# Performance work log

Hardware: AMD Instinct MI355X
Metric: run time of the kernel (lower is better)

## Reference

```python
import jax, jax.numpy as jnp
import numpy as np

N = 100000
E = 1600000
EPS = 1e-5


def setup_inputs() -> dict:
    key = jax.random.key(0)
    ks = jax.random.split(key, 6)
    x = jax.random.normal(ks[0], (N, 128), dtype=jnp.float32)
    edge_index = jax.random.randint(ks[1], (2, E), 0, N, dtype=jnp.int64)
    # Glorot-ish scaled weights
    W1 = jax.random.normal(ks[2], (128, 128), dtype=jnp.float32) * (1.0 / np.sqrt(128))
    b1 = jnp.zeros((128,), dtype=jnp.float32)
    gamma = jnp.ones((128,), dtype=jnp.float32)
    beta = jnp.zeros((128,), dtype=jnp.float32)
    W2 = jax.random.normal(ks[3], (64, 128), dtype=jnp.float32) * (1.0 / np.sqrt(128))
    b2 = jnp.zeros((64,), dtype=jnp.float32)
    return {"x": x, "edge_index": edge_index, "W1": W1, "b1": b1,
            "gamma": gamma, "beta": beta, "W2": W2, "b2": b2}


def _gcn_conv(x, W, b, src, dst, norm, n):
    # x: [N, Fin], W: [Fout, Fin] -> h: [N, Fout]
    h = x @ W.T
    msg = h[src] * norm[:, None]               # [E+N, Fout] gather + scale
    out = jax.ops.segment_sum(msg, dst, num_segments=n)  # scatter-add
    return out + b


def reference(x, edge_index, W1, b1, gamma, beta, W2, b2):
    n = x.shape[0]
    loop = jnp.arange(n, dtype=edge_index.dtype)
    src = jnp.concatenate([edge_index[0], loop])   # self-loops appended
    dst = jnp.concatenate([edge_index[1], loop])
    # symmetric normalization D^-1/2 A D^-1/2 (degree at destination)
    deg = jax.ops.segment_sum(jnp.ones_like(dst, dtype=x.dtype), dst, num_segments=n)
    dis = jnp.where(deg > 0, jax.lax.rsqrt(deg), 0.0)
    norm = dis[src] * dis[dst]

    h = _gcn_conv(x, W1, b1, src, dst, norm, n)
    # BatchNorm1d (training mode: biased batch statistics over nodes)
    mean = jnp.mean(h, axis=0)
    var = jnp.mean((h - mean) ** 2, axis=0)
    h = (h - mean) * jax.lax.rsqrt(var + EPS) * gamma + beta
    h = jax.nn.relu(h)
    out = _gcn_conv(h, W2, b2, src, dst, norm, n)
    return out
```

## Files before the change

kernel.cpp:

```cpp
#include <hip/hip_runtime.h>


#define SHIFT 8
#define BSZ   256
#define CHUNK 4096
#define EPT   (CHUNK/256)
#define NBMAX 1024

typedef short bf16x8 __attribute__((ext_vector_type(8)));
typedef float f32x4  __attribute__((ext_vector_type(4)));

__device__ __forceinline__ unsigned short f2bf(float f) {
    unsigned int u = __float_as_uint(f);
    unsigned int r = (u + 0x7FFFu + ((u >> 16) & 1u)) >> 16;
    return (unsigned short)r;
}
__device__ __forceinline__ float bf2f(unsigned short h) {
    return __uint_as_float(((unsigned int)h) << 16);
}
__device__ __forceinline__ unsigned int pack2bf(float a, float b) {
    return (unsigned int)f2bf(a) | ((unsigned int)f2bf(b) << 16);
}
__device__ __forceinline__ void fma4(float4& acc, float s, const float4& w) {
    acc.x += s * w.x; acc.y += s * w.y; acc.z += s * w.z; acc.w += s * w.w;
}

__device__ __forceinline__ void split2(float a, float b, unsigned int& hi, unsigned int& lo) {
    unsigned int ua = __float_as_uint(a), ub = __float_as_uint(b);
    unsigned int ha = ua & 0xFFFF0000u,  hb = ub & 0xFFFF0000u;
    hi = (ha >> 16) | hb;
    float la = a - __uint_as_float(ha);
    float lb = b - __uint_as_float(hb);
    lo = (__float_as_uint(la) >> 16) | (__float_as_uint(lb) & 0xFFFF0000u);
}

__global__ void k_detect(const int* __restrict__ ei32, int* __restrict__ flag) {
    if (threadIdx.x == 0 && blockIdx.x == 0) {
        int o = 0;
        for (int q = 0; q < 16; ++q) o |= ei32[2 * q + 1];
        flag[0] = (o == 0) ? 1 : 0;
    }
}

__global__ __launch_bounds__(256) void k_hist(const void* __restrict__ eiv,
                                              const int* __restrict__ flag,
                                              int* __restrict__ gcnt,
                                              int E, int N, int NB) {
    __shared__ int h[NBMAX];
    int t = threadIdx.x;
    for (int u = t; u < NB; u += 256) h[u] = 0;
    __syncthreads();
    int base = blockIdx.x * CHUNK;
    int f = flag[0];
    const long long* e64 = (const long long*)eiv;
    const int*       e32 = (const int*)eiv;
#pragma unroll
    for (int r = 0; r < EPT; ++r) {
        int e = base + r * 256 + t;
        if (e < E) {
            int s, d;
            if (f) { s = (int)e64[e]; d = (int)e64[E + e]; }
            else   { s = e32[e];      d = e32[E + e]; }
            if ((unsigned)s < (unsigned)N && (unsigned)d < (unsigned)N)
                atomicAdd(&h[d >> SHIFT], 1);
        }
    }
    __syncthreads();
    for (int u = t; u < NB; u += 256) {
        int c = h[u];
        if (c) atomicAdd(&gcnt[u], c);
    }
}

__global__ void k_scan(const int* __restrict__ gcnt, int* __restrict__ gbase,
                       int* __restrict__ gcur, int NB) {
    __shared__ int sh[1024];
    int t = threadIdx.x;
    int v = (t < NB) ? gcnt[t] : 0;
    sh[t] = v;
    __syncthreads();
    for (int off = 1; off < 1024; off <<= 1) {
        int x = sh[t];
        int y = (t >= off) ? sh[t - off] : 0;
        __syncthreads();
        sh[t] = x + y;
        __syncthreads();
    }
    if (t < NB) {
        int ex = sh[t] - v;
        gbase[t] = ex;
        gcur[t]  = ex;
    }
    if (t == 0) gbase[NB] = sh[1023];
}

__global__ __launch_bounds__(256) void k_scatter(const void* __restrict__ eiv,
                                                 const int* __restrict__ flag,
                                                 int* __restrict__ gcur,
                                                 unsigned int* __restrict__ ebuf,
                                                 int E, int N, int NB) {
    __shared__ int lcnt[NBMAX];
    __shared__ int lbase[NBMAX];
    int t = threadIdx.x;
    for (int u = t; u < NB; u += 256) lcnt[u] = 0;
    __syncthreads();
    int base = blockIdx.x * CHUNK;
    int f = flag[0];
    const long long* e64 = (const long long*)eiv;
    const int*       e32 = (const int*)eiv;
    unsigned int ent[EPT];
    int bk[EPT];
    int off[EPT];
#pragma unroll
    for (int r = 0; r < EPT; ++r) {
        int e = base + r * 256 + t;
        bk[r] = -1;
        if (e < E) {
            int s, d;
            if (f) { s = (int)e64[e]; d = (int)e64[E + e]; }
            else   { s = e32[e];      d = e32[E + e]; }
            if ((unsigned)s < (unsigned)N && (unsigned)d < (unsigned)N) {
                int b = d >> SHIFT;
                bk[r]  = b;
                off[r] = atomicAdd(&lcnt[b], 1);
                ent[r] = ((unsigned int)(d & (BSZ - 1)) << 24) | (unsigned int)s;
            }
        }
    }
    __syncthreads();
    for (int u = t; u < NB; u += 256) {
        int c = lcnt[u];
        lbase[u] = c ? atomicAdd(&gcur[u], c) : 0;
    }
    __syncthreads();
#pragma unroll
    for (int r = 0; r < EPT; ++r)
        if (bk[r] >= 0) ebuf[(size_t)lbase[bk[r]] + off[r]] = ent[r];
}

__global__ __launch_bounds__(256) void k_fine(const unsigned int* __restrict__ ebuf,
                                              const int* __restrict__ gbase,
                                              int* __restrict__ cnt,
                                              float* __restrict__ dis,
                                              int* __restrict__ rowptr,
                                              int* __restrict__ elist, int N) {
    __shared__ int lc[BSZ];
    __shared__ int ls[BSZ];
    int t = threadIdx.x;
    int b = blockIdx.x;
    int start = gbase[b], end = gbase[b + 1];
    int m = end - start;
    lc[t] = 0;
    __syncthreads();
    for (int j = t; j < m; j += 256)
        atomicAdd(&lc[ebuf[start + j] >> 24], 1);
    __syncthreads();
    int v = lc[t];
    ls[t] = v;
    __syncthreads();
    for (int off = 1; off < BSZ; off <<= 1) {
        int x = ls[t];
        int y = (t >= off) ? ls[t - off] : 0;
        __syncthreads();
        ls[t] = x + y;
        __syncthreads();
    }
    int ex = ls[t] - v;
    int i = (b << SHIFT) + t;
    if (i < N) {
        cnt[i]    = v;
        dis[i]    = rsqrtf((float)v + 1.0f);
        rowptr[i] = start + ex;
    }
    lc[t] = ex;
    __syncthreads();
    for (int j = t; j < m; j += 256) {
        unsigned int e = ebuf[start + j];
        int p = atomicAdd(&lc[e >> 24], 1);
        elist[start + p] = (int)(e & 0xFFFFFFu);
    }
}

__global__ __launch_bounds__(256) void k_transpose(const float* __restrict__ src,
                                                   float* __restrict__ dst, int O) {
    int idx = blockIdx.x * 256 + threadIdx.x;
    if (idx >= O * 128) return;
    int k = idx & 127, o = idx >> 7;
    dst[k * O + o] = src[o * 128 + k];
}

__global__ __launch_bounds__(256) void k_prepw(const float* __restrict__ W,
                                               uint4* __restrict__ Whi,
                                               uint4* __restrict__ Wlo, int NT) {
    int idx = blockIdx.x * 256 + threadIdx.x;
    if (idx >= NT * 4 * 64) return;
    int lane = idx & 63, kt = (idx >> 6) & 3, nt = idx >> 8;
    int o = nt * 16 + (lane & 15);
    int k0 = kt * 32 + (lane >> 4) * 8;
    const float* p = W + (size_t)o * 128 + k0;
    unsigned int h[4], l[4];
#pragma unroll
    for (int pr = 0; pr < 4; ++pr) split2(p[2 * pr], p[2 * pr + 1], h[pr], l[pr]);
    Whi[idx] = make_uint4(h[0], h[1], h[2], h[3]);
    Wlo[idx] = make_uint4(l[0], l[1], l[2], l[3]);
}

__global__ __launch_bounds__(256) void k_gemm1(const float* __restrict__ x,
                                               const uint4* __restrict__ Whi,
                                               const uint4* __restrict__ Wlo,
                                               const float* __restrict__ dis,
                                               unsigned short* __restrict__ h1b, int N) {
    __shared__ uint4 Ahi[1024];
    __shared__ uint4 Alo[1024];
    int t = threadIdx.x;
    int n0 = blockIdx.x * 64;
    for (int s = t; s < 1024; s += 256) {
        int lane = s & 63, kt = (s >> 6) & 3, c = s >> 8;
        int row = n0 + c * 16 + (lane & 15);
        int rr = min(row, N - 1);
        int k0 = kt * 32 + (lane >> 4) * 8;
        const float4* p = (const float4*)(x + (size_t)rr * 128 + k0);
        float4 u0 = p[0], u1 = p[1];
        unsigned int h0, h1, h2, h3, l0, l1, l2, l3;
        split2(u0.x, u0.y, h0, l0);
        split2(u0.z, u0.w, h1, l1);
        split2(u1.x, u1.y, h2, l2);
        split2(u1.z, u1.w, h3, l3);
        Ahi[s] = make_uint4(h0, h1, h2, h3);
        Alo[s] = make_uint4(l0, l1, l2, l3);
    }
    __syncthreads();
    int w = t >> 6, lane = t & 63;
    bf16x8 ah[4], al[4];
#pragma unroll
    for (int kt = 0; kt < 4; ++kt) {
        ah[kt] = ((const bf16x8*)Ahi)[(w * 4 + kt) * 64 + lane];
        al[kt] = ((const bf16x8*)Alo)[(w * 4 + kt) * 64 + lane];
    }
    f32x4 acc[8];
#pragma unroll
    for (int nt = 0; nt < 8; ++nt) {
        acc[nt] = (f32x4)(0.f);
#pragma unroll
        for (int kt = 0; kt < 4; ++kt) {
            bf16x8 bh = ((const bf16x8*)Whi)[(nt * 4 + kt) * 64 + lane];
            bf16x8 bl = ((const bf16x8*)Wlo)[(nt * 4 + kt) * 64 + lane];
            acc[nt] = __builtin_amdgcn_mfma_f32_16x16x32_bf16(ah[kt], bh, acc[nt], 0, 0, 0);
            acc[nt] = __builtin_amdgcn_mfma_f32_16x16x32_bf16(ah[kt], bl, acc[nt], 0, 0, 0);
            acc[nt] = __builtin_amdgcn_mfma_f32_16x16x32_bf16(al[kt], bh, acc[nt], 0, 0, 0);
        }
    }
    int r0 = n0 + w * 16 + (lane >> 4) * 4;
    float dv[4];
#pragma unroll
    for (int r = 0; r < 4; ++r) {
        int row = r0 + r;
        dv[r] = (row < N) ? dis[row] : 0.f;
    }
#pragma unroll
    for (int nt = 0; nt < 8; ++nt) {
        int col = nt * 16 + (lane & 15);
#pragma unroll
        for (int r = 0; r < 4; ++r) {
            int row = r0 + r;
            if (row < N) h1b[(size_t)row * 128 + col] = f2bf(dv[r] * acc[nt][r]);
        }
    }
}

__global__ __launch_bounds__(256) void k_agg1(const unsigned int* __restrict__ h1b,
                                              const float* __restrict__ dis,
                                              const int* __restrict__ rowptr,
                                              const int* __restrict__ cnt,
                                              const int* __restrict__ elist,
                                              float* __restrict__ agg1, int N) {
    int lane = threadIdx.x & 63;
    int i = blockIdx.x * 4 + (threadIdx.x >> 6);
    if (i >= N) return;
    float accx = 0.f, accy = 0.f;
    int base = rowptr[i], c = cnt[i];
    int j = 0;
    for (; j + 8 <= c; j += 8) {
        int ss[8];
#pragma unroll
        for (int r = 0; r < 8; ++r) ss[r] = elist[base + j + r];
        unsigned int vv[8];
#pragma unroll
        for (int r = 0; r < 8; ++r) vv[r] = h1b[(size_t)ss[r] * 64 + lane];
#pragma unroll
        for (int r = 0; r < 8; ++r) {
            accx += bf2f((unsigned short)(vv[r] & 0xFFFF));
            accy += bf2f((unsigned short)(vv[r] >> 16));
        }
    }
    for (; j < c; ++j) {
        int s = elist[base + j];
        unsigned int v = h1b[(size_t)s * 64 + lane];
        accx += bf2f((unsigned short)(v & 0xFFFF));
        accy += bf2f((unsigned short)(v >> 16));
    }
    float di = dis[i];
    unsigned int sv = h1b[(size_t)i * 64 + lane];
    float2 r;
    r.x = di * (accx + bf2f((unsigned short)(sv & 0xFFFF)));
    r.y = di * (accy + bf2f((unsigned short)(sv >> 16)));
    ((float2*)agg1)[(size_t)i * 64 + lane] = r;
}

__global__ __launch_bounds__(256) void k_bnstats(const float* __restrict__ agg1,
                                                 float* __restrict__ stats, int N) {
    int t = threadIdx.x;
    int f = t & 127, half = t >> 7;
    float s = 0.f, sq = 0.f;
    int stride = gridDim.x * 2;
    for (int r = blockIdx.x * 2 + half; r < N; r += stride) {
        float v = agg1[r * 128 + f];
        s += v; sq += v * v;
    }
    __shared__ float ls[256], lq[256];
    ls[t] = s; lq[t] = sq;
    __syncthreads();
    if (t < 128) {
        atomicAdd(&stats[f], ls[t] + ls[t + 128]);
        atomicAdd(&stats[128 + f], lq[t] + lq[t + 128]);
    }
}

__global__ void k_bnfin(float* __restrict__ stats, const float* __restrict__ gamma,
                        const float* __restrict__ beta, int N) {
    int f = threadIdx.x;
    if (f >= 128) return;
    float invN = 1.0f / (float)N;
    float mean = stats[f] * invN;
    float var = stats[128 + f] * invN - mean * mean;
    var = fmaxf(var, 0.f);
    float inv = rsqrtf(var + 1e-5f);
    float sc = gamma[f] * inv;
    stats[256 + f] = sc;
    stats[384 + f] = beta[f] - mean * sc;
}

__global__ __launch_bounds__(256) void k_gemm2(const float* __restrict__ agg1,
                                               const float* __restrict__ WT2,
                                               const float* __restrict__ stats,
                                               const float* __restrict__ dis,
                                               uint2* __restrict__ h2b, int N) {
    int t = threadIdx.x;
    int q = t & 15, g = t >> 4;
    int n0 = blockIdx.x * 64 + g * 4;
    int m0 = min(n0 + 0, N - 1), m1 = min(n0 + 1, N - 1);
    int m2 = min(n0 + 2, N - 1), m3 = min(n0 + 3, N - 1);
    const float4* ar0 = (const float4*)agg1 + (size_t)m0 * 32;
    const float4* ar1 = (const float4*)agg1 + (size_t)m1 * 32;
    const float4* ar2 = (const float4*)agg1 + (size_t)m2 * 32;
    const float4* ar3 = (const float4*)agg1 + (size_t)m3 * 32;
    const float4* wt = (const float4*)WT2;
    const float4* st = (const float4*)stats;
    float4 acc0 = make_float4(0.f, 0.f, 0.f, 0.f), acc1 = acc0, acc2 = acc0, acc3 = acc0;
    for (int kq = 0; kq < 32; ++kq) {
        float4 sc = st[64 + kq], sh = st[96 + kq];
        float4 a0 = ar0[kq], a1 = ar1[kq], a2 = ar2[kq], a3 = ar3[kq];
        float4 r0, r1, r2, r3;
        r0.x = fmaxf(a0.x * sc.x + sh.x, 0.f); r0.y = fmaxf(a0.y * sc.y + sh.y, 0.f);
        r0.z = fmaxf(a0.z * sc.z + sh.z, 0.f); r0.w = fmaxf(a0.w * sc.w + sh.w, 0.f);
        r1.x = fmaxf(a1.x * sc.x + sh.x, 0.f); r1.y = fmaxf(a1.y * sc.y + sh.y, 0.f);
        r1.z = fmaxf(a1.z * sc.z + sh.z, 0.f); r1.w = fmaxf(a1.w * sc.w + sh.w, 0.f);
        r2.x = fmaxf(a2.x * sc.x + sh.x, 0.f); r2.y = fmaxf(a2.y * sc.y + sh.y, 0.f);
        r2.z = fmaxf(a2.z * sc.z + sh.z, 0.f); r2.w = fmaxf(a2.w * sc.w + sh.w, 0.f);
        r3.x = fmaxf(a3.x * sc.x + sh.x, 0.f); r3.y = fmaxf(a3.y * sc.y + sh.y, 0.f);
        r3.z = fmaxf(a3.z * sc.z + sh.z, 0.f); r3.w = fmaxf(a3.w * sc.w + sh.w, 0.f);
        float4 w0 = wt[(4 * kq + 0) * 16 + q];
        float4 w1 = wt[(4 * kq + 1) * 16 + q];
        float4 w2 = wt[(4 * kq + 2) * 16 + q];
        float4 w3 = wt[(4 * kq + 3) * 16 + q];
        fma4(acc0, r0.x, w0); fma4(acc0, r0.y, w1); fma4(acc0, r0.z, w2); fma4(acc0, r0.w, w3);
        fma4(acc1, r1.x, w0); fma4(acc1, r1.y, w1); fma4(acc1, r1.z, w2); fma4(acc1, r1.w, w3);
        fma4(acc2, r2.x, w0); fma4(acc2, r2.y, w1); fma4(acc2, r2.z, w2); fma4(acc2, r2.w, w3);
        fma4(acc3, r3.x, w0); fma4(acc3, r3.y, w1); fma4(acc3, r3.z, w2); fma4(acc3, r3.w, w3);
    }
    float d0 = dis[m0], d1 = dis[m1], d2 = dis[m2], d3 = dis[m3];
    if (n0 + 0 < N) h2b[(size_t)(n0 + 0) * 16 + q] = make_uint2(pack2bf(d0 * acc0.x, d0 * acc0.y), pack2bf(d0 * acc0.z, d0 * acc0.w));
    if (n0 + 1 < N) h2b[(size_t)(n0 + 1) * 16 + q] = make_uint2(pack2bf(d1 * acc1.x, d1 * acc1.y), pack2bf(d1 * acc1.z, d1 * acc1.w));
    if (n0 + 2 < N) h2b[(size_t)(n0 + 2) * 16 + q] = make_uint2(pack2bf(d2 * acc2.x, d2 * acc2.y), pack2bf(d2 * acc2.z, d2 * acc2.w));
    if (n0 + 3 < N) h2b[(size_t)(n0 + 3) * 16 + q] = make_uint2(pack2bf(d3 * acc3.x, d3 * acc3.y), pack2bf(d3 * acc3.z, d3 * acc3.w));
}

__global__ __launch_bounds__(256) void k_agg2(const unsigned short* __restrict__ h2b,
                                              const float* __restrict__ dis,
                                              const int* __restrict__ rowptr,
                                              const int* __restrict__ cnt,
                                              const int* __restrict__ elist,
                                              const float* __restrict__ b2,
                                              float* __restrict__ out, int N) {
    int lane = threadIdx.x & 63;
    int i = blockIdx.x * 4 + (threadIdx.x >> 6);
    if (i >= N) return;
    float acc = 0.f;
    int base = rowptr[i], c = cnt[i];
    int j = 0;
    for (; j + 8 <= c; j += 8) {
        int ss[8];
#pragma unroll
        for (int r = 0; r < 8; ++r) ss[r] = elist[base + j + r];
        unsigned short vv[8];
#pragma unroll
        for (int r = 0; r < 8; ++r) vv[r] = h2b[(size_t)ss[r] * 64 + lane];
#pragma unroll
        for (int r = 0; r < 8; ++r) acc += bf2f(vv[r]);
    }
    for (; j < c; ++j) {
        int s = elist[base + j];
        acc += bf2f(h2b[(size_t)s * 64 + lane]);
    }
    float di = dis[i];
    float self = bf2f(h2b[(size_t)i * 64 + lane]);
    out[(size_t)i * 64 + lane] = di * (acc + self) + b2[lane];
}

extern "C" void kernel_launch(void* const* d_in, const int* in_sizes, int n_in,
                              void* d_out, int out_size, void* d_ws, size_t ws_size,
                              hipStream_t stream) {
    const float* x     = (const float*)d_in[0];
    const void*  ei    = d_in[1];
    const float* W1    = (const float*)d_in[2];
    const float* gamma = (const float*)d_in[4];
    const float* beta  = (const float*)d_in[5];
    const float* W2    = (const float*)d_in[6];
    const float* b2    = (const float*)d_in[7];
    float* out = (float*)d_out;

    int N = in_sizes[0] / 128;
    int E = in_sizes[1] / 2;
    int NB = (N + BSZ - 1) >> SHIFT;

    size_t Na = ((size_t)N + 3) & ~(size_t)3;
    size_t Ea = ((size_t)E + 3) & ~(size_t)3;
    int*   cnt    = (int*)d_ws;
    int*   rowptr = cnt + Na;
    int*   gcnt   = rowptr + Na;
    int*   gbase  = gcnt + 1024;
    int*   gcur   = gbase + 1028;
    int*   flagA  = gcur + 1024;
    float* stats  = (float*)(flagA + 4);
    float* dis    = stats + 512;
    int*   elist  = (int*)(dis + Na);
    unsigned int* h1b = (unsigned int*)(elist + Ea);
    float* agg1   = (float*)(h1b + Na * 64);
    unsigned int* ebuf = (unsigned int*)agg1;
    float* WT2    = agg1 + Na * 128;
    uint4* Whi1   = (uint4*)(WT2 + 128 * 64);
    uint4* Wlo1   = Whi1 + 2048;
    unsigned int* h2b = h1b;

    hipMemsetAsync(gcnt, 0, 1024 * sizeof(int), stream);
    hipMemsetAsync(stats, 0, 512 * sizeof(float), stream);

    k_detect<<<1, 64, 0, stream>>>((const int*)ei, flagA);

    int gC    = (E + CHUNK - 1) / CHUNK;
    int gG1   = (N + 63) / 64;
    int gG2   = (N + 63) / 64;
    int gAgg  = (N + 3) / 4;

    k_prepw<<<8, 256, 0, stream>>>(W1, Whi1, Wlo1, 8);
    k_transpose<<<32, 256, 0, stream>>>(W2, WT2, 64);
    k_hist<<<gC, 256, 0, stream>>>(ei, flagA, gcnt, E, N, NB);
    k_scan<<<1, 1024, 0, stream>>>(gcnt, gbase, gcur, NB);
    k_scatter<<<gC, 256, 0, stream>>>(ei, flagA, gcur, ebuf, E, N, NB);
    k_fine<<<NB, 256, 0, stream>>>(ebuf, gbase, cnt, dis, rowptr, elist, N);
    k_gemm1<<<gG1, 256, 0, stream>>>(x, Whi1, Wlo1, dis, (unsigned short*)h1b, N);
    k_agg1<<<gAgg, 256, 0, stream>>>(h1b, dis, rowptr, cnt, elist, agg1, N);
    k_bnstats<<<500, 256, 0, stream>>>(agg1, stats, N);
    k_bnfin<<<1, 128, 0, stream>>>(stats, gamma, beta, N);
    k_gemm2<<<gG2, 256, 0, stream>>>(agg1, WT2, stats, dis, (uint2*)h2b, N);
    k_agg2<<<gAgg, 256, 0, stream>>>((const unsigned short*)h2b, dis, rowptr, cnt, elist, b2, out, N);
}
```

Baseline: 459.3 us.

## Move second GEMM to split-bf16 MFMA and unroll aggregation gathers by 16

Replaces the scalar FP32 second GEMM with a bf16 MFMA version that stages BN+ReLU-applied activations into shared memory as hi/lo bf16 splits. It reuses the prepw weight-split kernel for W2 and computes three MFMAs per tile to keep near-FP32 accuracy. Both aggregation kernels now issue 16 independent gathers per iteration instead of 8, to raise memory-level parallelism. The cost is extra register pressure, more shared memory per block, and the overhead of the hi/lo split.

Measured after the change: 418.4 us. 1.1x faster.

```diff
diff --git a/kernel.cpp b/kernel.cpp
--- a/kernel.cpp
+++ b/kernel.cpp
@@ -18,13 +18,6 @@
 __device__ __forceinline__ float bf2f(unsigned short h) {
     return __uint_as_float(((unsigned int)h) << 16);
 }
-__device__ __forceinline__ unsigned int pack2bf(float a, float b) {
-    return (unsigned int)f2bf(a) | ((unsigned int)f2bf(b) << 16);
-}
-__device__ __forceinline__ void fma4(float4& acc, float s, const float4& w) {
-    acc.x += s * w.x; acc.y += s * w.y; acc.z += s * w.z; acc.w += s * w.w;
-}
-
 __device__ __forceinline__ void split2(float a, float b, unsigned int& hi, unsigned int& lo) {
     unsigned int ua = __float_as_uint(a), ub = __float_as_uint(b);
     unsigned int ha = ua & 0xFFFF0000u,  hb = ub & 0xFFFF0000u;
@@ -179,14 +172,6 @@
         int p = atomicAdd(&lc[e >> 24], 1);
         elist[start + p] = (int)(e & 0xFFFFFFu);
     }
-}
-
-__global__ __launch_bounds__(256) void k_transpose(const float* __restrict__ src,
-                                                   float* __restrict__ dst, int O) {
-    int idx = blockIdx.x * 256 + threadIdx.x;
-    if (idx >= O * 128) return;
-    int k = idx & 127, o = idx >> 7;
-    dst[k * O + o] = src[o * 128 + k];
 }
 
 __global__ __launch_bounds__(256) void k_prepw(const float* __restrict__ W,
@@ -280,7 +265,20 @@
     float accx = 0.f, accy = 0.f;
     int base = rowptr[i], c = cnt[i];
     int j = 0;
-    for (; j + 8 <= c; j += 8) {
+    for (; j + 16 <= c; j += 16) {
+        int ss[16];
+#pragma unroll
+        for (int r = 0; r < 16; ++r) ss[r] = elist[base + j + r];
+        unsigned int vv[16];
+#pragma unroll
+        for (int r = 0; r < 16; ++r) vv[r] = h1b[(size_t)ss[r] * 64 + lane];
+#pragma unroll
+        for (int r = 0; r < 16; ++r) {
+            accx += bf2f((unsigned short)(vv[r] & 0xFFFF));
+            accy += bf2f((unsigned short)(vv[r] >> 16));
+        }
+    }
+    if (j + 8 <= c) {
         int ss[8];
 #pragma unroll
         for (int r = 0; r < 8; ++r) ss[r] = elist[base + j + r];
@@ -292,6 +290,7 @@
             accx += bf2f((unsigned short)(vv[r] & 0xFFFF));
             accy += bf2f((unsigned short)(vv[r] >> 16));
         }
+        j += 8;
     }
     for (; j < c; ++j) {
         int s = elist[base + j];
@@ -341,48 +340,78 @@
 }
 
 __global__ __launch_bounds__(256) void k_gemm2(const float* __restrict__ agg1,
-                                               const float* __restrict__ WT2,
+                                               const uint4* __restrict__ Whi,
+                                               const uint4* __restrict__ Wlo,
                                                const float* __restrict__ stats,
                                                const float* __restrict__ dis,
-                                               uint2* __restrict__ h2b, int N) {
-    int t = threadIdx.x;
-    int q = t & 15, g = t >> 4;
-    int n0 = blockIdx.x * 64 + g * 4;
-    int m0 = min(n0 + 0, N - 1), m1 = min(n0 + 1, N - 1);
-    int m2 = min(n0 + 2, N - 1), m3 = min(n0 + 3, N - 1);
-    const float4* ar0 = (const float4*)agg1 + (size_t)m0 * 32;
-    const float4* ar1 = (const float4*)agg1 + (size_t)m1 * 32;
-    const float4* ar2 = (const float4*)agg1 + (size_t)m2 * 32;
-    const float4* ar3 = (const float4*)agg1 + (size_t)m3 * 32;
-    const float4* wt = (const float4*)WT2;
+                                               unsigned short* __restrict__ h2b, int N) {
+    __shared__ uint4 Ahi[1024];
+    __shared__ uint4 Alo[1024];
+    int t = threadIdx.x;
+    int n0 = blockIdx.x * 64;
     const float4* st = (const float4*)stats;
-    float4 acc0 = make_float4(0.f, 0.f, 0.f, 0.f), acc1 = acc0, acc2 = acc0, acc3 = acc0;
-    for (int kq = 0; kq < 32; ++kq) {
-        float4 sc = st[64 + kq], sh = st[96 + kq];
-        float4 a0 = ar0[kq], a1 = ar1[kq], a2 = ar2[kq], a3 = ar3[kq];
-        float4 r0, r1, r2, r3;
-        r0.x = fmaxf(a0.x * sc.x + sh.x, 0.f); r0.y = fmaxf(a0.y * sc.y + sh.y, 0.f);
-        r0.z = fmaxf(a0.z * sc.z + sh.z, 0.f); r0.w = fmaxf(a0.w * sc.w + sh.w, 0.f);
-        r1.x = fmaxf(a1.x * sc.x + sh.x, 0.f); r1.y = fmaxf(a1.y * sc.y + sh.y, 0.f);
-        r1.z = fmaxf(a1.z * sc.z + sh.z, 0.f); r1.w = fmaxf(a1.w * sc.w + sh.w, 0.f);
-        r2.x = fmaxf(a2.x * sc.x + sh.x, 0.f); r2.y = fmaxf(a2.y * sc.y + sh.y, 0.f);
-        r2.z = fmaxf(a2.z * sc.z + sh.z, 0.f); r2.w = fmaxf(a2.w * sc.w + sh.w, 0.f);
-        r3.x = fmaxf(a3.x * sc.x + sh.x, 0.f); r3.y = fmaxf(a3.y * sc.y + sh.y, 0.f);
-        r3.z = fmaxf(a3.z * sc.z + sh.z, 0.f); r3.w = fmaxf(a3.w * sc.w + sh.w, 0.f);
-        float4 w0 = wt[(4 * kq + 0) * 16 + q];
-        float4 w1 = wt[(4 * kq + 1) * 16 + q];
-        float4 w2 = wt[(4 * kq + 2) * 16 + q];
-        float4 w3 = wt[(4 * kq + 3) * 16 + q];
-        fma4(acc0, r0.x, w0); fma4(acc0, r0.y, w1); fma4(acc0, r0.z, w2); fma4(acc0, r0.w, w3);
-        fma4(acc1, r1.x, w0); fma4(acc1, r1.y, w1); fma4(acc1, r1.z, w2); fma4(acc1, r1.w, w3);
-        fma4(acc2, r2.x, w0); fma4(acc2, r2.y, w1); fma4(acc2, r2.z, w2); fma4(acc2, r2.w, w3);
-        fma4(acc3, r3.x, w0); fma4(acc3, r3.y, w1); fma4(acc3, r3.z, w2); fma4(acc3, r3.w, w3);
-    }
-    float d0 = dis[m0], d1 = dis[m1], d2 = dis[m2], d3 = dis[m3];
-    if (n0 + 0 < N) h2b[(size_t)(n0 + 0) * 16 + q] = make_uint2(pack2bf(d0 * acc0.x, d0 * acc0.y), pack2bf(d0 * acc0.z, d0 * acc0.w));
-    if (n0 + 1 < N) h2b[(size_t)(n0 + 1) * 16 + q] = make_uint2(pack2bf(d1 * acc1.x, d1 * acc1.y), pack2bf(d1 * acc1.z, d1 * acc1.w));
-    if (n0 + 2 < N) h2b[(size_t)(n0 + 2) * 16 + q] = make_uint2(pack2bf(d2 * acc2.x, d2 * acc2.y), pack2bf(d2 * acc2.z, d2 * acc2.w));
-    if (n0 + 3 < N) h2b[(size_t)(n0 + 3) * 16 + q] = make_uint2(pack2bf(d3 * acc3.x, d3 * acc3.y), pack2bf(d3 * acc3.z, d3 * acc3.w));
+    for (int s = t; s < 1024; s += 256) {
+        int lane = s & 63, kt = (s >> 6) & 3, c = s >> 8;
+        int row = n0 + c * 16 + (lane & 15);
+        int rr = min(row, N - 1);
+        int k0 = kt * 32 + (lane >> 4) * 8;
+        const float4* p = (const float4*)(agg1 + (size_t)rr * 128 + k0);
+        float4 a0 = p[0], a1 = p[1];
+        float4 c0 = st[64 + (k0 >> 2)], c1 = st[65 + (k0 >> 2)];
+        float4 s0 = st[96 + (k0 >> 2)], s1 = st[97 + (k0 >> 2)];
+        float v0 = fmaxf(a0.x * c0.x + s0.x, 0.f);
+        float v1 = fmaxf(a0.y * c0.y + s0.y, 0.f);
+        float v2 = fmaxf(a0.z * c0.z + s0.z, 0.f);
+        float v3 = fmaxf(a0.w * c0.w + s0.w, 0.f);
+        float v4 = fmaxf(a1.x * c1.x + s1.x, 0.f);
+        float v5 = fmaxf(a1.y * c1.y + s1.y, 0.f);
+        float v6 = fmaxf(a1.z * c1.z + s1.z, 0.f);
+        float v7 = fmaxf(a1.w * c1.w + s1.w, 0.f);
+        unsigned int h0, h1, h2, h3, l0, l1, l2, l3;
+        split2(v0, v1, h0, l0);
+        split2(v2, v3, h1, l1);
+        split2(v4, v5, h2, l2);
+        split2(v6, v7, h3, l3);
+        Ahi[s] = make_uint4(h0, h1, h2, h3);
+        Alo[s] = make_uint4(l0, l1, l2, l3);
+    }
+    __syncthreads();
+    int w = t >> 6, lane = t & 63;
+    bf16x8 ah[4], al[4];
+#pragma unroll
+    for (int kt = 0; kt < 4; ++kt) {
+        ah[kt] = ((const bf16x8*)Ahi)[(w * 4 + kt) * 64 + lane];
+        al[kt] = ((const bf16x8*)Alo)[(w * 4 + kt) * 64 + lane];
+    }
+    f32x4 acc[4];
+#pragma unroll
+    for (int nt = 0; nt < 4; ++nt) {
+        acc[nt] = (f32x4)(0.f);
+#pragma unroll
+        for (int kt = 0; kt < 4; ++kt) {
+            bf16x8 bh = ((const bf16x8*)Whi)[(nt * 4 + kt) * 64 + lane];
+            bf16x8 bl = ((const bf16x8*)Wlo)[(nt * 4 + kt) * 64 + lane];
+            acc[nt] = __builtin_amdgcn_mfma_f32_16x16x32_bf16(ah[kt], bh, acc[nt], 0, 0, 0);
+            acc[nt] = __builtin_amdgcn_mfma_f32_16x16x32_bf16(ah[kt], bl, acc[nt], 0, 0, 0);
+            acc[nt] = __builtin_amdgcn_mfma_f32_16x16x32_bf16(al[kt], bh, acc[nt], 0, 0, 0);
+        }
+    }
+    int r0 = n0 + w * 16 + (lane >> 4) * 4;
+    float dv[4];
+#pragma unroll
+    for (int r = 0; r < 4; ++r) {
+        int row = r0 + r;
+        dv[r] = (row < N) ? dis[row] : 0.f;
+    }
+#pragma unroll
+    for (int nt = 0; nt < 4; ++nt) {
+        int col = nt * 16 + (lane & 15);
+#pragma unroll
+        for (int r = 0; r < 4; ++r) {
+            int row = r0 + r;
+            if (row < N) h2b[(size_t)row * 64 + col] = f2bf(dv[r] * acc[nt][r]);
+        }
+    }
 }
 
 __global__ __launch_bounds__(256) void k_agg2(const unsigned short* __restrict__ h2b,
@@ -398,7 +427,17 @@
     float acc = 0.f;
     int base = rowptr[i], c = cnt[i];
     int j = 0;
-    for (; j + 8 <= c; j += 8) {
+    for (; j + 16 <= c; j += 16) {
+        int ss[16];
+#pragma unroll
+        for (int r = 0; r < 16; ++r) ss[r] = elist[base + j + r];
+        unsigned short vv[16];
+#pragma unroll
+        for (int r = 0; r < 16; ++r) vv[r] = h2b[(size_t)ss[r] * 64 + lane];
+#pragma unroll
+        for (int r = 0; r < 16; ++r) acc += bf2f(vv[r]);
+    }
+    if (j + 8 <= c) {
         int ss[8];
 #pragma unroll
         for (int r = 0; r < 8; ++r) ss[r] = elist[base + j + r];
@@ -407,6 +446,7 @@
         for (int r = 0; r < 8; ++r) vv[r] = h2b[(size_t)ss[r] * 64 + lane];
 #pragma unroll
         for (int r = 0; r < 8; ++r) acc += bf2f(vv[r]);
+        j += 8;
     }
     for (; j < c; ++j) {
         int s = elist[base + j];
@@ -447,9 +487,10 @@
     unsigned int* h1b = (unsigned int*)(elist + Ea);
     float* agg1   = (float*)(h1b + Na * 64);
     unsigned int* ebuf = (unsigned int*)agg1;
-    float* WT2    = agg1 + Na * 128;
-    uint4* Whi1   = (uint4*)(WT2 + 128 * 64);
+    uint4* Whi1   = (uint4*)(agg1 + Na * 128);
     uint4* Wlo1   = Whi1 + 2048;
+    uint4* Whi2   = Wlo1 + 2048;
+    uint4* Wlo2   = Whi2 + 1024;
     unsigned int* h2b = h1b;
 
     hipMemsetAsync(gcnt, 0, 1024 * sizeof(int), stream);
@@ -459,11 +500,10 @@
 
     int gC    = (E + CHUNK - 1) / CHUNK;
     int gG1   = (N + 63) / 64;
-    int gG2   = (N + 63) / 64;
     int gAgg  = (N + 3) / 4;
 
     k_prepw<<<8, 256, 0, stream>>>(W1, Whi1, Wlo1, 8);
-    k_transpose<<<32, 256, 0, stream>>>(W2, WT2, 64);
+    k_prepw<<<4, 256, 0, stream>>>(W2, Whi2, Wlo2, 4);
     k_hist<<<gC, 256, 0, stream>>>(ei, flagA, gcnt, E, N, NB);
     k_scan<<<1, 1024, 0, stream>>>(gcnt, gbase, gcur, NB);
     k_scatter<<<gC, 256, 0, stream>>>(ei, flagA, gcur, ebuf, E, N, NB);
@@ -472,6 +512,6 @@
     k_agg1<<<gAgg, 256, 0, stream>>>(h1b, dis, rowptr, cnt, elist, agg1, N);
     k_bnstats<<<500, 256, 0, stream>>>(agg1, stats, N);
     k_bnfin<<<1, 128, 0, stream>>>(stats, gamma, beta, N);
-    k_gemm2<<<gG2, 256, 0, stream>>>(agg1, WT2, stats, dis, (uint2*)h2b, N);
+    k_gemm2<<<gG1, 256, 0, stream>>>(agg1, Whi2, Wlo2, stats, dis, (unsigned short*)h2b, N);
     k_agg2<<<gAgg, 256, 0, stream>>>((const unsigned short*)h2b, dis, rowptr, cnt, elist, b2, out, N);
 }
```
